# Kernel optimization log

Measured on AMD Instinct MI355X. Metric: run time of the kernel, lower is better.

## Reference

```python
import jax, jax.numpy as jnp
import numpy as np

H = 1024  # hidden_size
I = 1024  # input_size

def _xavier(key, shape):
    fan_in, fan_out = shape
    a = jnp.sqrt(6.0 / (fan_in + fan_out))
    return jax.random.uniform(key, shape, jnp.float32, -a, a)

def setup_inputs() -> dict:
    key = jax.random.key(0)
    ks = jax.random.split(key, 9)
    x = jax.random.normal(ks[0], (64, 512, I), dtype=jnp.float32)
    W_xi = _xavier(ks[1], (I, H)); W_hi = _xavier(ks[2], (H, H))
    W_xf = _xavier(ks[3], (I, H)); W_hf = _xavier(ks[4], (H, H))
    W_xc = _xavier(ks[5], (I, H)); W_hc = _xavier(ks[6], (H, H))
    W_xo = _xavier(ks[7], (I, H)); W_ho = _xavier(ks[8], (H, H))
    b_i = jnp.zeros((H,), jnp.float32); b_f = jnp.zeros((H,), jnp.float32)
    b_c = jnp.zeros((H,), jnp.float32); b_o = jnp.zeros((H,), jnp.float32)
    return dict(x=x, W_xi=W_xi, W_hi=W_hi, b_i=b_i, W_xf=W_xf, W_hf=W_hf, b_f=b_f,
                W_xc=W_xc, W_hc=W_hc, b_c=b_c, W_xo=W_xo, W_ho=W_ho, b_o=b_o)

def reference(x, W_xi, W_hi, b_i, W_xf, W_hf, b_f, W_xc, W_hc, b_c, W_xo, W_ho, b_o):
    B, T, _ = x.shape
    # precompute input projections for all gates in one batched GEMM each
    # shapes: [B, T, H]
    xi = jnp.einsum('bti,ih->bth', x, W_xi) + b_i
    xf = jnp.einsum('bti,ih->bth', x, W_xf) + b_f
    xc = jnp.einsum('bti,ih->bth', x, W_xc) + b_c
    xo = jnp.einsum('bti,ih->bth', x, W_xo) + b_o
    # time-major for scan: [T, B, H]
    xs = (jnp.swapaxes(xi, 0, 1), jnp.swapaxes(xf, 0, 1),
          jnp.swapaxes(xc, 0, 1), jnp.swapaxes(xo, 0, 1))
    h0 = jnp.zeros((B, W_hi.shape[0]), x.dtype)
    c0 = jnp.zeros_like(h0)

    def step(carry, inp):
        h, c = carry
        xi_t, xf_t, xc_t, xo_t = inp
        i_t = jax.nn.sigmoid(xi_t + h @ W_hi)
        f_t = jax.nn.sigmoid(xf_t + h @ W_hf)
        c_hat = jnp.tanh(xc_t + h @ W_hc)
        c_new = f_t * c + i_t * c_hat
        o_t = jax.nn.sigmoid(xo_t + h @ W_ho)
        h_new = o_t * jnp.tanh(c_new)
        return (h_new, c_new), h_new

    (h_T, c_T), hs = jax.lax.scan(step, (h0, c0), xs)
    outputs = jnp.swapaxes(hs, 0, 1)  # [B, T, H]
    return outputs, (h_T, c_T)
```

## Files before the change

kernel.cpp:

```cpp
#include <hip/hip_runtime.h>

typedef __attribute__((ext_vector_type(8))) __bf16 bf16x8;
typedef __attribute__((ext_vector_type(4))) __bf16 bf16x4;
typedef __attribute__((ext_vector_type(4))) float f32x4;
typedef unsigned long long u64;

#define OUT_HT (64ll*512*1024)
#define OUT_CT (OUT_HT + 64*1024)

__global__ void convert_x(const float4* __restrict__ in, bf16x4* __restrict__ outp) {
    int i = blockIdx.x * 256 + threadIdx.x;
    float4 v = in[i];
    bf16x4 o;
    o[0] = (__bf16)v.x; o[1] = (__bf16)v.y; o[2] = (__bf16)v.z; o[3] = (__bf16)v.w;
    outp[i] = o;
}

__global__ void build_w(const float* __restrict__ Wxi, const float* __restrict__ Whi,
                        const float* __restrict__ Wxf, const float* __restrict__ Whf,
                        const float* __restrict__ Wxc, const float* __restrict__ Whc,
                        const float* __restrict__ Wxo, const float* __restrict__ Who,
                        __bf16* __restrict__ wf) {
    int idx = blockIdx.x * 256 + threadIdx.x;
    int k = idx >> 12, n = idx & 4095;
    int h = n >> 2, g = n & 3;
    const float* W;
    if (k < 1024) W = (g == 0 ? Wxi : g == 1 ? Wxf : g == 2 ? Wxc : Wxo);
    else          W = (g == 0 ? Whi : g == 1 ? Whf : g == 2 ? Whc : Who);
    float v = W[(k & 1023) * 1024 + h];
    int kc = k >> 5, quad = (k >> 3) & 3, j = k & 7;
    int ng = n >> 4, l = quad * 16 + (n & 15);
    wf[((((ng * 64) + kc) * 64 + l) << 3) + j] = (__bf16)v;
}

__global__ void __launch_bounds__(256, 1) lstm_rnn(
    const __bf16* __restrict__ xbf,
    const __bf16* __restrict__ wf,
    const float* __restrict__ bi, const float* __restrict__ bfg,
    const float* __restrict__ bc, const float* __restrict__ bo,
    __bf16* __restrict__ ring,
    int* __restrict__ bar,
    float* __restrict__ out)
{
    const int blk = blockIdx.x, tid = threadIdx.x;
    const int wave = tid >> 6, lane = tid & 63;
    const int l15 = lane & 15, quad = lane >> 4;

    bf16x8 wfrag[64];
    const bf16x8* wsrc = (const bf16x8*)(wf + (size_t)blk * 64 * 64 * 8);
    #pragma unroll
    for (int kc = 0; kc < 64; ++kc)
        wfrag[kc] = wsrc[kc * 64 + lane];

    __threadfence();
    __syncthreads();
    if (tid == 0)
        __hip_atomic_fetch_add(&bar[(blk & 63) * 16], 1,
                               __ATOMIC_RELAXED, __HIP_MEMORY_SCOPE_AGENT);
    if (tid < 64) {
        while (__hip_atomic_load(&bar[tid * 16], __ATOMIC_RELAXED,
                                 __HIP_MEMORY_SCOPE_AGENT) < 4)
            __builtin_amdgcn_s_sleep(2);
    }
    __syncthreads();

    if (tid < 64)
        __hip_atomic_store(((u64*)ring) + tid * 256 + blk, 0ULL,
                           __ATOMIC_RELAXED, __HIP_MEMORY_SCOPE_AGENT);
    __builtin_amdgcn_s_waitcnt(0);
    __syncthreads();
    if (tid == 0)
        __hip_atomic_fetch_add(&bar[(blk & 63) * 16], 1,
                               __ATOMIC_RELAXED, __HIP_MEMORY_SCOPE_AGENT);

    const int pb = tid >> 2, phl = tid & 3;
    const int hcol = blk * 4 + phl;
    const float bias_i = bi[hcol], bias_f = bfg[hcol],
                bias_c = bc[hcol], bias_o = bo[hcol];
    float c_reg = 0.f;

    __shared__ float gates[64 * 17];
    __shared__ u64 hstage[64];

    const int brow = wave * 16 + l15;
    const __bf16* xrow_base = xbf + ((size_t)brow * 512) * 1024 + quad * 8;

    for (int t = 0; t < 512; ++t) {
        f32x4 acc0a = {0.f,0.f,0.f,0.f}, acc0b = {0.f,0.f,0.f,0.f};
        const __bf16* xrow = xrow_base + (size_t)t * 1024;
        #pragma unroll
        for (int kc = 0; kc < 16; ++kc) {
            bf16x8 a0 = *(const bf16x8*)(xrow + (2*kc) * 32);
            bf16x8 a1 = *(const bf16x8*)(xrow + (2*kc+1) * 32);
            acc0a = __builtin_amdgcn_mfma_f32_16x16x32_bf16(a0, wfrag[2*kc],   acc0a, 0,0,0);
            acc0b = __builtin_amdgcn_mfma_f32_16x16x32_bf16(a1, wfrag[2*kc+1], acc0b, 0,0,0);
        }

        const int target = 4 * (t + 2);
        if (tid < 64) {
            while (__hip_atomic_load(&bar[tid * 16], __ATOMIC_RELAXED,
                                     __HIP_MEMORY_SCOPE_AGENT) < target)
                __builtin_amdgcn_s_sleep(2);
        }
        __syncthreads();

        f32x4 acc1a = {0.f,0.f,0.f,0.f}, acc1b = {0.f,0.f,0.f,0.f};
        const __bf16* hrow = ring + (size_t)(t & 63) * 65536 + brow * 1024 + quad * 8;
        #pragma unroll
        for (int kc = 0; kc < 16; ++kc) {
            bf16x8 a0 = *(const bf16x8*)(hrow + (2*kc) * 32);
            bf16x8 a1 = *(const bf16x8*)(hrow + (2*kc+1) * 32);
            acc1a = __builtin_amdgcn_mfma_f32_16x16x32_bf16(a0, wfrag[32+2*kc],   acc1a, 0,0,0);
            acc1b = __builtin_amdgcn_mfma_f32_16x16x32_bf16(a1, wfrag[32+2*kc+1], acc1b, 0,0,0);
        }

        #pragma unroll
        for (int r = 0; r < 4; ++r)
            gates[(wave * 16 + quad * 4 + r) * 17 + l15] =
                acc0a[r] + acc0b[r] + acc1a[r] + acc1b[r];
        __syncthreads();
        {
            float gi = gates[pb * 17 + phl * 4 + 0] + bias_i;
            float gf = gates[pb * 17 + phl * 4 + 1] + bias_f;
            float gc = gates[pb * 17 + phl * 4 + 2] + bias_c;
            float go = gates[pb * 17 + phl * 4 + 3] + bias_o;
            float it = 1.f / (1.f + __expf(-gi));
            float ft = 1.f / (1.f + __expf(-gf));
            float ch = tanhf(gc);
            float ot = 1.f / (1.f + __expf(-go));
            c_reg = ft * c_reg + it * ch;
            float hn = ot * tanhf(c_reg);
            ((__bf16*)&hstage[pb])[phl] = (__bf16)hn;
            __builtin_nontemporal_store(hn, &out[((size_t)pb * 512 + t) * 1024 + hcol]);
            if (t == 511) {
                __builtin_nontemporal_store(hn,    &out[OUT_HT + pb * 1024 + hcol]);
                __builtin_nontemporal_store(c_reg, &out[OUT_CT + pb * 1024 + hcol]);
            }
        }
        __syncthreads();
        if (t < 511) {
            if (tid < 64) {
                u64 hv = hstage[tid];
                __hip_atomic_store(((u64*)(ring + (size_t)((t + 1) & 63) * 65536))
                                       + tid * 256 + blk,
                                   hv, __ATOMIC_RELAXED, __HIP_MEMORY_SCOPE_AGENT);
            }
            __builtin_amdgcn_s_waitcnt(0);
            __syncthreads();
            if (tid == 0)
                __hip_atomic_fetch_add(&bar[(blk & 63) * 16], 1,
                                       __ATOMIC_RELAXED, __HIP_MEMORY_SCOPE_AGENT);
        }
    }
}

extern "C" void kernel_launch(void* const* d_in, const int* in_sizes, int n_in,
                              void* d_out, int out_size, void* d_ws, size_t ws_size,
                              hipStream_t stream) {
    const float* x   = (const float*)d_in[0];
    const float* Wxi = (const float*)d_in[1];
    const float* Whi = (const float*)d_in[2];
    const float* bi  = (const float*)d_in[3];
    const float* Wxf = (const float*)d_in[4];
    const float* Whf = (const float*)d_in[5];
    const float* bfg = (const float*)d_in[6];
    const float* Wxc = (const float*)d_in[7];
    const float* Whc = (const float*)d_in[8];
    const float* bc  = (const float*)d_in[9];
    const float* Wxo = (const float*)d_in[10];
    const float* Who = (const float*)d_in[11];
    const float* bo  = (const float*)d_in[12];
    float* out = (float*)d_out;

    char* ws = (char*)d_ws;
    __bf16* wcombF = (__bf16*)ws;
    __bf16* xbf    = (__bf16*)(ws + (16ll << 20));
    __bf16* ring   = (__bf16*)(ws + (80ll << 20));
    int*    bar    = (int*)(ws + (88ll << 20));

    hipMemsetAsync(bar, 0, 64 * 64, stream);

    hipLaunchKernelGGL(convert_x, dim3(32768), dim3(256), 0, stream,
                       (const float4*)x, (bf16x4*)xbf);
    hipLaunchKernelGGL(build_w, dim3(32768), dim3(256), 0, stream,
                       Wxi, Whi, Wxf, Whf, Wxc, Whc, Wxo, Who, wcombF);

    hipLaunchKernelGGL(lstm_rnn, dim3(256), dim3(256), 0, stream,
                       xbf, wcombF, bi, bfg, bc, bo, ring, bar, out);
}
```

Before: 6.540 ms.

## Partition batch into four independent groups with per-group barriers

Repartitions the 256 blocks into 4 batch groups of 64 blocks, each handling 16 batch rows and 16 hidden columns, so that each step's barrier spans only 64 blocks instead of all 256. Each wave now holds weights for a different 4-column slice, and the h ring buffer is split per group. Global output stores are moved after the barrier signal to shorten the critical path. In exchange, each block's MFMA work now covers only 16 rows per wave across distinct column slices, and the gate layout in shared memory changes.

Measured after the change: 6.224 ms. 1.05x faster.

```diff
diff --git a/kernel.cpp b/kernel.cpp
--- a/kernel.cpp
+++ b/kernel.cpp
@@ -40,14 +40,16 @@
     const float* __restrict__ bc, const float* __restrict__ bo,
     __bf16* __restrict__ ring,
     int* __restrict__ bar,
+    int* __restrict__ gbar,
     float* __restrict__ out)
 {
     const int blk = blockIdx.x, tid = threadIdx.x;
+    const int g = blk >> 6, bl = blk & 63;
     const int wave = tid >> 6, lane = tid & 63;
     const int l15 = lane & 15, quad = lane >> 4;
 
     bf16x8 wfrag[64];
-    const bf16x8* wsrc = (const bf16x8*)(wf + (size_t)blk * 64 * 64 * 8);
+    const bf16x8* wsrc = (const bf16x8*)(wf + (size_t)(bl * 4 + wave) * (64 * 64 * 8));
     #pragma unroll
     for (int kc = 0; kc < 64; ++kc)
         wfrag[kc] = wsrc[kc * 64 + lane];
@@ -64,26 +66,32 @@
     }
     __syncthreads();
 
-    if (tid < 64)
-        __hip_atomic_store(((u64*)ring) + tid * 256 + blk, 0ULL,
+    u64* ring64 = (u64*)ring;
+    const size_t gbase64 = (size_t)g * (64 * 4096);
+    if (tid < 64) {
+        int batch = tid >> 2, part = tid & 3;
+        __hip_atomic_store(ring64 + gbase64 + batch * 256 + bl * 4 + part, 0ULL,
                            __ATOMIC_RELAXED, __HIP_MEMORY_SCOPE_AGENT);
+    }
     __builtin_amdgcn_s_waitcnt(0);
     __syncthreads();
+    int* gcnt = gbar + (g * 16 + (bl & 15)) * 16;
     if (tid == 0)
-        __hip_atomic_fetch_add(&bar[(blk & 63) * 16], 1,
-                               __ATOMIC_RELAXED, __HIP_MEMORY_SCOPE_AGENT);
-
-    const int pb = tid >> 2, phl = tid & 3;
-    const int hcol = blk * 4 + phl;
+        __hip_atomic_fetch_add(gcnt, 1, __ATOMIC_RELAXED, __HIP_MEMORY_SCOPE_AGENT);
+
+    const int pb = tid >> 4, phl = tid & 15;
+    const int hcol = bl * 16 + phl;
+    const int bglob = g * 16 + pb;
     const float bias_i = bi[hcol], bias_f = bfg[hcol],
                 bias_c = bc[hcol], bias_o = bo[hcol];
     float c_reg = 0.f;
 
-    __shared__ float gates[64 * 17];
+    __shared__ float gates[16 * 65];
     __shared__ u64 hstage[64];
 
-    const int brow = wave * 16 + l15;
-    const __bf16* xrow_base = xbf + ((size_t)brow * 512) * 1024 + quad * 8;
+    const __bf16* xrow_base = xbf + ((size_t)(g * 16 + l15) * 512) * 1024 + quad * 8;
+    const __bf16* ringg = ring + (size_t)g * (64 * 16384);
+    int* pollp = (tid < 16) ? (gbar + (g * 16 + tid) * 16) : gbar;
 
     for (int t = 0; t < 512; ++t) {
         f32x4 acc0a = {0.f,0.f,0.f,0.f}, acc0b = {0.f,0.f,0.f,0.f};
@@ -96,16 +104,16 @@
             acc0b = __builtin_amdgcn_mfma_f32_16x16x32_bf16(a1, wfrag[2*kc+1], acc0b, 0,0,0);
         }
 
-        const int target = 4 * (t + 2);
-        if (tid < 64) {
-            while (__hip_atomic_load(&bar[tid * 16], __ATOMIC_RELAXED,
+        const int target = 4 * (t + 1);
+        if (tid < 16) {
+            while (__hip_atomic_load(pollp, __ATOMIC_RELAXED,
                                      __HIP_MEMORY_SCOPE_AGENT) < target)
                 __builtin_amdgcn_s_sleep(2);
         }
         __syncthreads();
 
         f32x4 acc1a = {0.f,0.f,0.f,0.f}, acc1b = {0.f,0.f,0.f,0.f};
-        const __bf16* hrow = ring + (size_t)(t & 63) * 65536 + brow * 1024 + quad * 8;
+        const __bf16* hrow = ringg + (size_t)(t & 63) * 16384 + l15 * 1024 + quad * 8;
         #pragma unroll
         for (int kc = 0; kc < 16; ++kc) {
             bf16x8 a0 = *(const bf16x8*)(hrow + (2*kc) * 32);
@@ -116,40 +124,42 @@
 
         #pragma unroll
         for (int r = 0; r < 4; ++r)
-            gates[(wave * 16 + quad * 4 + r) * 17 + l15] =
+            gates[(quad * 4 + r) * 65 + wave * 16 + l15] =
                 acc0a[r] + acc0b[r] + acc1a[r] + acc1b[r];
         __syncthreads();
-        {
-            float gi = gates[pb * 17 + phl * 4 + 0] + bias_i;
-            float gf = gates[pb * 17 + phl * 4 + 1] + bias_f;
-            float gc = gates[pb * 17 + phl * 4 + 2] + bias_c;
-            float go = gates[pb * 17 + phl * 4 + 3] + bias_o;
-            float it = 1.f / (1.f + __expf(-gi));
-            float ft = 1.f / (1.f + __expf(-gf));
-            float ch = tanhf(gc);
-            float ot = 1.f / (1.f + __expf(-go));
-            c_reg = ft * c_reg + it * ch;
-            float hn = ot * tanhf(c_reg);
-            ((__bf16*)&hstage[pb])[phl] = (__bf16)hn;
-            __builtin_nontemporal_store(hn, &out[((size_t)pb * 512 + t) * 1024 + hcol]);
-            if (t == 511) {
-                __builtin_nontemporal_store(hn,    &out[OUT_HT + pb * 1024 + hcol]);
-                __builtin_nontemporal_store(c_reg, &out[OUT_CT + pb * 1024 + hcol]);
-            }
-        }
+
+        float gi = gates[pb * 65 + phl * 4 + 0] + bias_i;
+        float gf = gates[pb * 65 + phl * 4 + 1] + bias_f;
+        float gc = gates[pb * 65 + phl * 4 + 2] + bias_c;
+        float go = gates[pb * 65 + phl * 4 + 3] + bias_o;
+        float it = 1.f / (1.f + __expf(-gi));
+        float ft = 1.f / (1.f + __expf(-gf));
+        float ch = tanhf(gc);
+        float ot = 1.f / (1.f + __expf(-go));
+        c_reg = ft * c_reg + it * ch;
+        float hn = ot * tanhf(c_reg);
+        ((__bf16*)&hstage[pb * 4 + (phl >> 2)])[phl & 3] = (__bf16)hn;
         __syncthreads();
+
         if (t < 511) {
             if (tid < 64) {
                 u64 hv = hstage[tid];
-                __hip_atomic_store(((u64*)(ring + (size_t)((t + 1) & 63) * 65536))
-                                       + tid * 256 + blk,
+                int batch = tid >> 2, part = tid & 3;
+                __hip_atomic_store(ring64 + gbase64 + (size_t)((t + 1) & 63) * 4096
+                                       + batch * 256 + bl * 4 + part,
                                    hv, __ATOMIC_RELAXED, __HIP_MEMORY_SCOPE_AGENT);
             }
             __builtin_amdgcn_s_waitcnt(0);
             __syncthreads();
             if (tid == 0)
-                __hip_atomic_fetch_add(&bar[(blk & 63) * 16], 1,
-                                       __ATOMIC_RELAXED, __HIP_MEMORY_SCOPE_AGENT);
+                __hip_atomic_fetch_add(gcnt, 1, __ATOMIC_RELAXED,
+                                       __HIP_MEMORY_SCOPE_AGENT);
+        }
+
+        __builtin_nontemporal_store(hn, &out[((size_t)bglob * 512 + t) * 1024 + hcol]);
+        if (t == 511) {
+            __builtin_nontemporal_store(hn,    &out[OUT_HT + bglob * 1024 + hcol]);
+            __builtin_nontemporal_store(c_reg, &out[OUT_CT + bglob * 1024 + hcol]);
         }
     }
 }
@@ -177,8 +187,9 @@
     __bf16* xbf    = (__bf16*)(ws + (16ll << 20));
     __bf16* ring   = (__bf16*)(ws + (80ll << 20));
     int*    bar    = (int*)(ws + (88ll << 20));
-
-    hipMemsetAsync(bar, 0, 64 * 64, stream);
+    int*    gbar   = (int*)(ws + (88ll << 20) + 4096);
+
+    hipMemsetAsync(bar, 0, 8192, stream);
 
     hipLaunchKernelGGL(convert_x, dim3(32768), dim3(256), 0, stream,
                        (const float4*)x, (bf16x4*)xbf);
@@ -186,5 +197,5 @@
                        Wxi, Whi, Wxf, Whf, Wxc, Whc, Wxo, Who, wcombF);
 
     hipLaunchKernelGGL(lstm_rnn, dim3(256), dim3(256), 0, stream,
-                       xbf, wcombF, bi, bfg, bc, bo, ring, bar, out);
-}
+                       xbf, wcombF, bi, bfg, bc, bo, ring, bar, gbar, out);
+}
```
